# Optimization experiments

Hardware: AMD Instinct MI355X
Metric: run time of the kernel (lower is better)

The kernel has to match this reference:

```python
import jax, jax.numpy as jnp
import numpy as np

B, S, D = 4, 2048, 2048
H = 16
DH = D // H  # 128

def _rope_tables(seq_len, d_head, base=10000.0):
    inv_freq = 1.0 / (base ** (np.arange(0, d_head, 2, dtype=np.float32) / d_head))
    pos = np.arange(seq_len, dtype=np.float32)
    ang = pos[:, None] * inv_freq[None, :]  # (S, d_head/2)
    return jnp.asarray(np.cos(ang)), jnp.asarray(np.sin(ang))

def setup_inputs() -> dict:
    key = jax.random.key(0)
    ks = jax.random.split(key, 4)
    x = jax.random.normal(ks[0], (B, S, D), dtype=jnp.float32)
    rope_cos, rope_sin = _rope_tables(S, DH)
    # Linear params, scaled like torch default init (~1/sqrt(fan_in))
    Wqkv = jax.random.normal(ks[1], (D, 3 * D), dtype=jnp.float32) / np.sqrt(D)
    bqkv = jnp.zeros((3 * D,), dtype=jnp.float32)
    Wout = jax.random.normal(ks[2], (D, D), dtype=jnp.float32) / np.sqrt(D)
    bout = jnp.zeros((D,), dtype=jnp.float32)
    return {"x": x, "rope_cos": rope_cos, "rope_sin": rope_sin,
            "Wqkv": Wqkv, "bqkv": bqkv, "Wout": Wout, "bout": bout}

def _apply_rope(x, cos, sin):
    # x: (B, H, S, DH); cos/sin: (S, DH/2), broadcast over B,H
    x1 = x[..., 0::2]
    x2 = x[..., 1::2]
    out = jnp.stack([x1 * cos - x2 * sin, x1 * sin + x2 * cos], axis=-1)
    return out.reshape(*out.shape[:-2], -1)  # interleave back to (..., DH)

def reference(x, rope_cos, rope_sin, Wqkv, bqkv, Wout, bout):
    qkv = (x @ Wqkv + bqkv).reshape(B, S, 3, H, DH)
    qkv = jnp.transpose(qkv, (2, 0, 3, 1, 4))  # (3, B, H, S, DH)
    q, k, v = qkv[0], qkv[1], qkv[2]
    q = _apply_rope(q, rope_cos, rope_sin)
    k = _apply_rope(k, rope_cos, rope_sin)
    scale = 1.0 / np.sqrt(DH)
    scores = jnp.einsum('bhqd,bhkd->bhqk', q, k) * scale  # (B,H,S,S)
    causal = jnp.tril(jnp.ones((S, S), dtype=bool))
    scores = jnp.where(causal, scores, jnp.finfo(scores.dtype).min)
    attn = jax.nn.softmax(scores, axis=-1)
    out = jnp.einsum('bhqk,bhkd->bhqd', attn, v)  # (B,H,S,DH)
    out = jnp.transpose(out, (0, 2, 1, 3)).reshape(B, S, D)
    return out @ Wout + bout
```

## Files before the change

kernel.cpp:

```cpp
#include <hip/hip_runtime.h>
#include <hip/hip_bf16.h>
#include <math.h>

typedef __attribute__((ext_vector_type(8))) short bf16x8;
typedef __attribute__((ext_vector_type(4))) float f32x4;
typedef __attribute__((ext_vector_type(16))) float f32x16;
typedef __attribute__((ext_vector_type(8))) unsigned short u16x8;
typedef __attribute__((ext_vector_type(4))) unsigned short u16x4;

static constexpr int B = 4, S = 2048, D = 2048, H = 16, DH = 128;
static constexpr int N3 = 3 * D;
static constexpr int M = B * S;

__device__ __forceinline__ unsigned short f2bf(float f) {
  unsigned u = __float_as_uint(f);
  u += 0x7fffu + ((u >> 16) & 1u);
  return (unsigned short)(u >> 16);
}
__device__ __forceinline__ float bf2f(unsigned short b) {
  return __uint_as_float(((unsigned)b) << 16);
}

__global__ __launch_bounds__(256) void cvt_kernel(const float* __restrict__ in,
                                                  unsigned short* __restrict__ out) {
  size_t i = (size_t)blockIdx.x * 256 + threadIdx.x;
  f32x4 v = *(const f32x4*)(in + i * 4);
  u16x4 o;
  o[0] = f2bf(v[0]); o[1] = f2bf(v[1]); o[2] = f2bf(v[2]); o[3] = f2bf(v[3]);
  *(u16x4*)(out + i * 4) = o;
}

__global__ __launch_bounds__(256) void transpose_kernel(const float* __restrict__ W,
                                                        unsigned short* __restrict__ WT,
                                                        int K, int N) {
  __shared__ float t[32][33];
  int tx = threadIdx.x, ty = threadIdx.y;
  int n0 = blockIdx.x * 32, k0 = blockIdx.y * 32;
#pragma unroll
  for (int i = 0; i < 4; i++)
    t[ty + i * 8][tx] = W[(size_t)(k0 + ty + i * 8) * N + n0 + tx];
  __syncthreads();
#pragma unroll
  for (int i = 0; i < 4; i++)
    WT[(size_t)(n0 + ty + i * 8) * K + k0 + tx] = f2bf(t[tx][ty + i * 8]);
}

__device__ __forceinline__ void gload_lds(const void* g, void* l) {
  __builtin_amdgcn_global_load_lds((const __attribute__((address_space(1))) void*)g,
                                   (__attribute__((address_space(3))) void*)l, 16, 0, 0);
}

template <int EPI>
__global__ __launch_bounds__(512, 1) void gemm_bt(
    const unsigned short* __restrict__ A, const unsigned short* __restrict__ Bt,
    const float* __restrict__ bias, float* __restrict__ Cf,
    unsigned short* __restrict__ Qp, unsigned short* __restrict__ Kp,
    unsigned short* __restrict__ VTp, int Nn, int nbn) {
  __shared__ __align__(16) unsigned short lds[4 * 16384];
  constexpr int NT = 64;
  const int tid = threadIdx.x;
  const int l = tid & 63;
  const int w = tid >> 6;
  const int lr = l >> 4, lc = l & 15;
  const int wm = w >> 2, wn = w & 3;

  const int nwg = gridDim.x;
  const int cpx = nwg >> 3;
  const int wg = blockIdx.x;
  const int swz = (wg & 7) * cpx + (wg >> 3);
  const int bm = swz / nbn;
  const int bn = swz - bm * nbn;

  const unsigned short* Asrc[2];
  const unsigned short* Bsrc[2];
  int ldA[2], ldB[2];
#pragma unroll
  for (int i = 0; i < 2; i++) {
    const int gi = i * 512 + tid;
    const int r = gi >> 2, c = gi & 3;
    const int cs = c ^ ((r >> 1) & 3);
    Asrc[i] = A + (size_t)(bm * 256 + r) * 2048 + cs * 8;
    ldA[i] = gi * 8;
    Bsrc[i] = Bt + (size_t)(bn * 256 + r) * 2048 + cs * 8;
    ldB[i] = 8192 + gi * 8;
  }

  f32x4 acc[8][4];
#pragma unroll
  for (int m = 0; m < 8; m++)
#pragma unroll
    for (int n = 0; n < 4; n++) acc[m][n] = (f32x4)0.f;

  const int swzr = (lr ^ ((lc >> 1) & 3)) * 8;
  const int aoff = (wm * 128 + lc) * 32 + swzr;
  const int boff = 8192 + (wn * 64 + lc) * 32 + swzr;

#pragma unroll
  for (int t = 0; t < 3; t++) {
    unsigned short* sb = lds + t * 16384;
    gload_lds(Asrc[0] + t * 32, sb + ldA[0]);
    gload_lds(Asrc[1] + t * 32, sb + ldA[1]);
    gload_lds(Bsrc[0] + t * 32, sb + ldB[0]);
    gload_lds(Bsrc[1] + t * 32, sb + ldB[1]);
  }
  __builtin_amdgcn_sched_barrier(0);
  asm volatile("s_waitcnt vmcnt(8)" ::: "memory");
  __builtin_amdgcn_s_barrier();
  __builtin_amdgcn_sched_barrier(0);

  for (int kt = 0; kt < NT; kt++) {
    const unsigned short* buf = lds + (kt & 3) * 16384;
    unsigned short* sb = lds + ((kt + 3) & 3) * 16384;
    const bool stg = (kt + 3) < NT;
    const int ks = (kt + 3) * 32;
    bf16x8 a0[4], bb[4];
#pragma unroll
    for (int mf = 0; mf < 4; mf++) a0[mf] = *(const bf16x8*)(buf + aoff + mf * 512);
#pragma unroll
    for (int nf = 0; nf < 4; nf++) bb[nf] = *(const bf16x8*)(buf + boff + nf * 512);
    if (stg) { gload_lds(Asrc[0] + ks, sb + ldA[0]); gload_lds(Asrc[1] + ks, sb + ldA[1]); }
    __builtin_amdgcn_sched_barrier(0);
    __builtin_amdgcn_s_barrier();
    asm volatile("s_waitcnt lgkmcnt(0)" ::: "memory");
    __builtin_amdgcn_sched_barrier(0);
    __builtin_amdgcn_s_setprio(1);
#pragma unroll
    for (int m = 0; m < 4; m++)
#pragma unroll
      for (int n = 0; n < 4; n++)
        acc[m][n] = __builtin_amdgcn_mfma_f32_16x16x32_bf16(a0[m], bb[n], acc[m][n], 0, 0, 0);
    __builtin_amdgcn_s_setprio(0);
    __builtin_amdgcn_sched_barrier(0);
    __builtin_amdgcn_s_barrier();
    bf16x8 a1[4];
#pragma unroll
    for (int mf = 0; mf < 4; mf++) a1[mf] = *(const bf16x8*)(buf + aoff + (mf + 4) * 512);
    if (stg) { gload_lds(Bsrc[0] + ks, sb + ldB[0]); gload_lds(Bsrc[1] + ks, sb + ldB[1]); }
    __builtin_amdgcn_sched_barrier(0);
    __builtin_amdgcn_s_barrier();
    asm volatile("s_waitcnt lgkmcnt(0)" ::: "memory");
    __builtin_amdgcn_sched_barrier(0);
    __builtin_amdgcn_s_setprio(1);
#pragma unroll
    for (int m = 0; m < 4; m++)
#pragma unroll
      for (int n = 0; n < 4; n++)
        acc[m + 4][n] = __builtin_amdgcn_mfma_f32_16x16x32_bf16(a1[m], bb[n], acc[m + 4][n], 0, 0, 0);
    __builtin_amdgcn_s_setprio(0);
    __builtin_amdgcn_sched_barrier(0);
    if (kt + 3 < NT)      asm volatile("s_waitcnt vmcnt(8)" ::: "memory");
    else if (kt + 2 < NT) asm volatile("s_waitcnt vmcnt(4)" ::: "memory");
    else if (kt + 1 < NT) asm volatile("s_waitcnt vmcnt(0)" ::: "memory");
    __builtin_amdgcn_sched_barrier(0);
    __builtin_amdgcn_s_barrier();
    __builtin_amdgcn_sched_barrier(0);
  }

#pragma unroll
  for (int m = 0; m < 8; m++) {
#pragma unroll
    for (int n = 0; n < 4; n++) {
      const int col = bn * 256 + wn * 64 + n * 16 + lc;
      const float bv = bias[col];
#pragma unroll
      for (int r = 0; r < 4; r++) {
        const int row = bm * 256 + wm * 128 + m * 16 + lr * 4 + r;
        const float v = acc[m][n][r] + bv;
        if (EPI == 0) {
          const unsigned short ob = f2bf(v);
          const int b = row >> 11, s = row & 2047;
          const int which = col >> 11, within = col & 2047;
          const int h = within >> 7, d = within & 127;
          const size_t bh = (size_t)(b * H + h);
          if (which == 0)      Qp[(bh * S + s) * DH + d] = ob;
          else if (which == 1) Kp[(bh * S + s) * DH + d] = ob;
          else                 VTp[(bh * DH + d) * S + s] = ob;
        } else {
          Cf[(size_t)row * Nn + col] = v;
        }
      }
    }
  }
}

__global__ __launch_bounds__(256) void rope_kernel(unsigned short* __restrict__ T,
                                                   const float* __restrict__ cosT,
                                                   const float* __restrict__ sinT) {
  int t = blockIdx.x * 256 + threadIdx.x;
  int d8 = t & 15;
  int s = (t >> 4) & (S - 1);
  size_t off = (size_t)t * 8;
  u16x8 v = *(const u16x8*)(T + off);
  f32x4 c = *(const f32x4*)(cosT + (size_t)s * (DH / 2) + d8 * 4);
  f32x4 sn = *(const f32x4*)(sinT + (size_t)s * (DH / 2) + d8 * 4);
  u16x8 o;
#pragma unroll
  for (int j = 0; j < 4; j++) {
    float x1 = bf2f(v[2 * j]), x2 = bf2f(v[2 * j + 1]);
    o[2 * j]     = f2bf(x1 * c[j] - x2 * sn[j]);
    o[2 * j + 1] = f2bf(x1 * sn[j] + x2 * c[j]);
  }
  *(u16x8*)(T + off) = o;
}

__global__ __launch_bounds__(512, 1) void attn3_kernel(
    const unsigned short* __restrict__ Q, const unsigned short* __restrict__ Kt,
    const unsigned short* __restrict__ VT, unsigned short* __restrict__ O) {
  __shared__ __align__(16) unsigned short lK[2][32 * 128];
  __shared__ __align__(16) unsigned short lV[2][128 * 40];
  const int tid = threadIdx.x;
  const int w = tid >> 6;
  const int l = tid & 63;
  const int ql = l & 31;
  const int hi = l >> 5;
  const int j = blockIdx.x;
  const int bh = ((j >> 3) & 7) * 8 + (j & 7);
  const int pr = j >> 6;
  const int b = bh >> 4, h = bh & 15;
  const size_t base = (size_t)bh * S * DH;
  const float cl = 0.088388347648318447f * 1.44269504088896341f;

  const int kdst = (tid * 8) ^ (((tid >> 4) & 7) << 3);
  const unsigned short* Kgb = Kt + base;
  const int vdh = tid >> 2;
  const int vc = (tid & 3) * 8;
  const int vdst = vdh * 40 + vc;
  const unsigned short* Vgr = VT + ((size_t)bh * DH + vdh) * S;
  const int sfix = (ql & 7) << 3;

  for (int half = 0; half < 2; half++) {
    const int strip = half ? 7 - pr : pr;
    const int qw0 = strip * 256 + w * 32;

    bf16x8 qf[8];
    const unsigned short* qp = Q + base + (size_t)(qw0 + ql) * DH + hi * 8;
#pragma unroll
    for (int t = 0; t < 8; t++) qf[t] = *(const bf16x8*)(qp + t * 16);

    f32x16 acc[4];
#pragma unroll
    for (int mt = 0; mt < 4; mt++) acc[mt] = (f32x16)0.f;
    float m = -INFINITY, lsum = 0.f;

    const int ntb = 8 * (strip + 1);
    const int last = 8 * strip + w;

    {
      f32x4 kr = *(const f32x4*)(Kgb + tid * 8);
      f32x4 vr = *(const f32x4*)(Vgr + vc);
      *(f32x4*)(&lK[0][kdst]) = kr;
      *(f32x4*)(&lV[0][vdst]) = vr;
      __syncthreads();
    }

    for (int kb = 0; kb < ntb; kb++) {
      const int cur = kb & 1;
      const bool more = (kb + 1 < ntb);
      f32x4 kr, vr;
      if (more) {
        kr = *(const f32x4*)(Kgb + (size_t)(kb + 1) * 4096 + tid * 8);
        vr = *(const f32x4*)(Vgr + (kb + 1) * 32 + vc);
      }
      if (kb <= last) {
        const unsigned short* kbuf = lK[cur];
        const unsigned short* vbuf = lV[cur];
        f32x16 st0 = (f32x16)0.f, st1 = (f32x16)0.f;
#pragma unroll
        for (int t = 0; t < 4; t++) {
          bf16x8 k0 = *(const bf16x8*)(kbuf + ((ql * 128 + (2 * t) * 16 + 8 * hi) ^ sfix));
          bf16x8 k1 = *(const bf16x8*)(kbuf + ((ql * 128 + (2 * t + 1) * 16 + 8 * hi) ^ sfix));
          st0 = __builtin_amdgcn_mfma_f32_32x32x16_bf16(k0, qf[2 * t], st0, 0, 0, 0);
          st1 = __builtin_amdgcn_mfma_f32_32x32x16_bf16(k1, qf[2 * t + 1], st1, 0, 0, 0);
        }
        float sv[16];
#pragma unroll
        for (int r = 0; r < 16; r++) sv[r] = st0[r] + st1[r];
        if (kb == last) {
#pragma unroll
          for (int r = 0; r < 16; r++) {
            const int klocal = (r & 3) + 8 * (r >> 2) + 4 * hi;
            sv[r] = (klocal > ql) ? -INFINITY : sv[r];
          }
        }
        float smax = sv[0];
#pragma unroll
        for (int r = 1; r < 16; r++) smax = fmaxf(smax, sv[r]);
        smax = fmaxf(smax, __shfl_xor(smax, 32));

        float fr = 1.f;
        if (!__all((smax - m) * cl <= 8.0f)) {
          const float mn = fmaxf(m, smax);
          fr = exp2f((m - mn) * cl);
          m = mn;
#pragma unroll
          for (int mt = 0; mt < 4; mt++)
#pragma unroll
            for (int r = 0; r < 16; r++) acc[mt][r] *= fr;
        }
        float p[16];
        float ps = 0.f;
#pragma unroll
        for (int r = 0; r < 16; r++) {
          p[r] = exp2f((sv[r] - m) * cl);
          ps += p[r];
        }
        lsum = lsum * fr + ps + __shfl_xor(ps, 32);

        unsigned W[8];
#pragma unroll
        for (int qd = 0; qd < 4; qd++) {
          W[2 * qd]     = (unsigned)f2bf(p[4 * qd])     | ((unsigned)f2bf(p[4 * qd + 1]) << 16);
          W[2 * qd + 1] = (unsigned)f2bf(p[4 * qd + 2]) | ((unsigned)f2bf(p[4 * qd + 3]) << 16);
        }
#pragma unroll
        for (int t = 0; t < 2; t++) {
          const unsigned s0 = hi ? W[4 * t] : W[4 * t + 2];
          const unsigned s1 = hi ? W[4 * t + 1] : W[4 * t + 3];
          const unsigned r0 = __shfl_xor((int)s0, 32);
          const unsigned r1 = __shfl_xor((int)s1, 32);
          union { unsigned u[4]; bf16x8 v; } pf;
          if (hi == 0) { pf.u[0] = W[4 * t]; pf.u[1] = W[4 * t + 1]; pf.u[2] = r0; pf.u[3] = r1; }
          else         { pf.u[0] = r0; pf.u[1] = r1; pf.u[2] = W[4 * t + 2]; pf.u[3] = W[4 * t + 3]; }
#pragma unroll
          for (int mt = 0; mt < 4; mt++) {
            const bf16x8 vf = *(const bf16x8*)(vbuf + (mt * 32 + ql) * 40 + 16 * t + 8 * hi);
            acc[mt] = __builtin_amdgcn_mfma_f32_32x32x16_bf16(vf, pf.v, acc[mt], 0, 0, 0);
          }
        }
      }
      if (more) {
        *(f32x4*)(&lK[cur ^ 1][kdst]) = kr;
        *(f32x4*)(&lV[cur ^ 1][vdst]) = vr;
      }
      __syncthreads();
    }

    const float inv = 1.f / lsum;
    const int s_glob = qw0 + ql;
    unsigned short* op = O + ((size_t)(b * S + s_glob) * H + h) * DH;
#pragma unroll
    for (int mt = 0; mt < 4; mt++)
#pragma unroll
      for (int g = 0; g < 4; g++) {
        u16x4 ov;
#pragma unroll
        for (int jj = 0; jj < 4; jj++) ov[jj] = f2bf(acc[mt][4 * g + jj] * inv);
        *(u16x4*)(op + mt * 32 + 8 * g + 4 * hi) = ov;
      }
  }
}

extern "C" void kernel_launch(void* const* d_in, const int* in_sizes, int n_in,
                              void* d_out, int out_size, void* d_ws, size_t ws_size,
                              hipStream_t stream) {
  const float* x    = (const float*)d_in[0];
  const float* cosT = (const float*)d_in[1];
  const float* sinT = (const float*)d_in[2];
  const float* Wqkv = (const float*)d_in[3];
  const float* bqkv = (const float*)d_in[4];
  const float* Wout = (const float*)d_in[5];
  const float* bout = (const float*)d_in[6];

  char* ws = (char*)d_ws;
  unsigned short* xbf   = (unsigned short*)(ws);
  unsigned short* WqkvT = (unsigned short*)(ws + ((size_t)32 << 20));
  unsigned short* WoutT = (unsigned short*)(ws + ((size_t)56 << 20));
  unsigned short* VTb   = (unsigned short*)(ws + ((size_t)64 << 20));
  unsigned short* Qb = (unsigned short*)d_out;
  unsigned short* Kb = (unsigned short*)d_out + (size_t)M * D;
  unsigned short* Ob = xbf;

  cvt_kernel<<<M * D / 1024, 256, 0, stream>>>(x, xbf);
  transpose_kernel<<<dim3(N3 / 32, D / 32), dim3(32, 8), 0, stream>>>(Wqkv, WqkvT, D, N3);
  transpose_kernel<<<dim3(D / 32, D / 32), dim3(32, 8), 0, stream>>>(Wout, WoutT, D, D);
  gemm_bt<0><<<dim3((M / 256) * (N3 / 256)), 512, 0, stream>>>(xbf, WqkvT, bqkv, nullptr,
                                                               Qb, Kb, VTb, N3, N3 / 256);
  rope_kernel<<<(B * H * S * 16) / 256, 256, 0, stream>>>(Qb, cosT, sinT);
  rope_kernel<<<(B * H * S * 16) / 256, 256, 0, stream>>>(Kb, cosT, sinT);
  attn3_kernel<<<B * H * 4, 512, 0, stream>>>(Qb, Kb, VTb, Ob);
  gemm_bt<1><<<dim3((M / 256) * (D / 256)), 512, 0, stream>>>(Ob, WoutT, bout, (float*)d_out,
                                                              nullptr, nullptr, nullptr, D, D / 256);
}
```

Before: 502.2 us.

## Prefetch next k-tile LDS fragments into registers with ping-pong GEMM pipeline

Restructures the GEMM main loop so each iteration loads the next k-tile's A/B fragments from LDS into a second register set while MFMAs run on the current set. Partial lgkmcnt waits replace full drains, and the mid-iteration barriers are removed, leaving one barrier per tile. Global pointers are now advanced incrementally instead of recomputing offsets. This hides LDS read latency behind MFMA work at the cost of more VGPRs, and relies on fragile waitcnt and buffer-reuse ordering.

Result: faster. 490.0 us (-2.4%).

```diff
diff --git a/kernel.cpp b/kernel.cpp
--- a/kernel.cpp
+++ b/kernel.cpp
@@ -48,6 +48,60 @@
 __device__ __forceinline__ void gload_lds(const void* g, void* l) {
   __builtin_amdgcn_global_load_lds((const __attribute__((address_space(1))) void*)g,
                                    (__attribute__((address_space(3))) void*)l, 16, 0, 0);
+}
+
+template <bool NXT, bool STG, int VMN>
+__device__ __forceinline__ void gemm_tile(
+    const unsigned short* __restrict__ rb, unsigned short* __restrict__ sb,
+    bf16x8 (&CA)[8], bf16x8 (&CB)[4], bf16x8 (&NA)[8], bf16x8 (&NB)[4],
+    f32x4 (&acc)[8][4], int aoff, int boff,
+    const unsigned short*& pA0, const unsigned short*& pA1,
+    const unsigned short*& pB0, const unsigned short*& pB1,
+    int ldA0, int ldA1, int ldB0, int ldB1) {
+  if (NXT) {
+#pragma unroll
+    for (int mf = 0; mf < 4; mf++) NA[mf] = *(const bf16x8*)(rb + aoff + mf * 512);
+#pragma unroll
+    for (int nf = 0; nf < 4; nf++) NB[nf] = *(const bf16x8*)(rb + boff + nf * 512);
+  }
+  if (STG) { gload_lds(pA0, sb + ldA0); gload_lds(pA1, sb + ldA1); pA0 += 32; pA1 += 32; }
+  __builtin_amdgcn_sched_barrier(0);
+  if (NXT) asm volatile("s_waitcnt lgkmcnt(12)" ::: "memory");
+  else     asm volatile("s_waitcnt lgkmcnt(4)" ::: "memory");
+  __builtin_amdgcn_sched_barrier(0);
+  __builtin_amdgcn_s_setprio(1);
+#pragma unroll
+  for (int m = 0; m < 4; m++)
+#pragma unroll
+    for (int n = 0; n < 4; n++)
+      acc[m][n] = __builtin_amdgcn_mfma_f32_16x16x32_bf16(CA[m], CB[n], acc[m][n], 0, 0, 0);
+  __builtin_amdgcn_s_setprio(0);
+  __builtin_amdgcn_sched_barrier(0);
+  if (NXT) {
+#pragma unroll
+    for (int mf = 4; mf < 8; mf++) NA[mf] = *(const bf16x8*)(rb + aoff + mf * 512);
+  }
+  if (STG) { gload_lds(pB0, sb + ldB0); gload_lds(pB1, sb + ldB1); pB0 += 32; pB1 += 32; }
+  __builtin_amdgcn_sched_barrier(0);
+  if (NXT) asm volatile("s_waitcnt lgkmcnt(12)" ::: "memory");
+  else     asm volatile("s_waitcnt lgkmcnt(0)" ::: "memory");
+  __builtin_amdgcn_sched_barrier(0);
+  __builtin_amdgcn_s_setprio(1);
+#pragma unroll
+  for (int m = 0; m < 4; m++)
+#pragma unroll
+    for (int n = 0; n < 4; n++)
+      acc[m + 4][n] = __builtin_amdgcn_mfma_f32_16x16x32_bf16(CA[m + 4], CB[n], acc[m + 4][n], 0, 0, 0);
+  __builtin_amdgcn_s_setprio(0);
+  __builtin_amdgcn_sched_barrier(0);
+  if (VMN == 4) {
+    asm volatile("s_waitcnt vmcnt(4)" ::: "memory");
+    __builtin_amdgcn_s_barrier();
+  } else if (VMN == 0) {
+    asm volatile("s_waitcnt vmcnt(0)" ::: "memory");
+    __builtin_amdgcn_s_barrier();
+  }
+  __builtin_amdgcn_sched_barrier(0);
 }
 
 template <int EPI>
@@ -71,19 +125,15 @@
   const int bm = swz / nbn;
   const int bn = swz - bm * nbn;
 
-  const unsigned short* Asrc[2];
-  const unsigned short* Bsrc[2];
-  int ldA[2], ldB[2];
-#pragma unroll
-  for (int i = 0; i < 2; i++) {
-    const int gi = i * 512 + tid;
-    const int r = gi >> 2, c = gi & 3;
-    const int cs = c ^ ((r >> 1) & 3);
-    Asrc[i] = A + (size_t)(bm * 256 + r) * 2048 + cs * 8;
-    ldA[i] = gi * 8;
-    Bsrc[i] = Bt + (size_t)(bn * 256 + r) * 2048 + cs * 8;
-    ldB[i] = 8192 + gi * 8;
-  }
+  const int gi0 = tid, gi1 = 512 + tid;
+  const int r0 = gi0 >> 2, c0 = (gi0 & 3) ^ ((r0 >> 1) & 3);
+  const int r1 = gi1 >> 2, c1 = (gi1 & 3) ^ ((r1 >> 1) & 3);
+  const unsigned short* pA0 = A + (size_t)(bm * 256 + r0) * 2048 + c0 * 8;
+  const unsigned short* pA1 = A + (size_t)(bm * 256 + r1) * 2048 + c1 * 8;
+  const unsigned short* pB0 = Bt + (size_t)(bn * 256 + r0) * 2048 + c0 * 8;
+  const unsigned short* pB1 = Bt + (size_t)(bn * 256 + r1) * 2048 + c1 * 8;
+  const int ldA0 = gi0 * 8, ldA1 = gi1 * 8;
+  const int ldB0 = 8192 + gi0 * 8, ldB1 = 8192 + gi1 * 8;
 
   f32x4 acc[8][4];
 #pragma unroll
@@ -98,63 +148,44 @@
 #pragma unroll
   for (int t = 0; t < 3; t++) {
     unsigned short* sb = lds + t * 16384;
-    gload_lds(Asrc[0] + t * 32, sb + ldA[0]);
-    gload_lds(Asrc[1] + t * 32, sb + ldA[1]);
-    gload_lds(Bsrc[0] + t * 32, sb + ldB[0]);
-    gload_lds(Bsrc[1] + t * 32, sb + ldB[1]);
-  }
-  __builtin_amdgcn_sched_barrier(0);
-  asm volatile("s_waitcnt vmcnt(8)" ::: "memory");
+    gload_lds(pA0, sb + ldA0); gload_lds(pA1, sb + ldA1);
+    gload_lds(pB0, sb + ldB0); gload_lds(pB1, sb + ldB1);
+    pA0 += 32; pA1 += 32; pB0 += 32; pB1 += 32;
+  }
+  __builtin_amdgcn_sched_barrier(0);
+  asm volatile("s_waitcnt vmcnt(4)" ::: "memory");
   __builtin_amdgcn_s_barrier();
   __builtin_amdgcn_sched_barrier(0);
 
-  for (int kt = 0; kt < NT; kt++) {
-    const unsigned short* buf = lds + (kt & 3) * 16384;
-    unsigned short* sb = lds + ((kt + 3) & 3) * 16384;
-    const bool stg = (kt + 3) < NT;
-    const int ks = (kt + 3) * 32;
-    bf16x8 a0[4], bb[4];
-#pragma unroll
-    for (int mf = 0; mf < 4; mf++) a0[mf] = *(const bf16x8*)(buf + aoff + mf * 512);
-#pragma unroll
-    for (int nf = 0; nf < 4; nf++) bb[nf] = *(const bf16x8*)(buf + boff + nf * 512);
-    if (stg) { gload_lds(Asrc[0] + ks, sb + ldA[0]); gload_lds(Asrc[1] + ks, sb + ldA[1]); }
-    __builtin_amdgcn_sched_barrier(0);
-    __builtin_amdgcn_s_barrier();
-    asm volatile("s_waitcnt lgkmcnt(0)" ::: "memory");
-    __builtin_amdgcn_sched_barrier(0);
-    __builtin_amdgcn_s_setprio(1);
-#pragma unroll
-    for (int m = 0; m < 4; m++)
-#pragma unroll
-      for (int n = 0; n < 4; n++)
-        acc[m][n] = __builtin_amdgcn_mfma_f32_16x16x32_bf16(a0[m], bb[n], acc[m][n], 0, 0, 0);
-    __builtin_amdgcn_s_setprio(0);
-    __builtin_amdgcn_sched_barrier(0);
-    __builtin_amdgcn_s_barrier();
-    bf16x8 a1[4];
-#pragma unroll
-    for (int mf = 0; mf < 4; mf++) a1[mf] = *(const bf16x8*)(buf + aoff + (mf + 4) * 512);
-    if (stg) { gload_lds(Bsrc[0] + ks, sb + ldB[0]); gload_lds(Bsrc[1] + ks, sb + ldB[1]); }
-    __builtin_amdgcn_sched_barrier(0);
-    __builtin_amdgcn_s_barrier();
-    asm volatile("s_waitcnt lgkmcnt(0)" ::: "memory");
-    __builtin_amdgcn_sched_barrier(0);
-    __builtin_amdgcn_s_setprio(1);
-#pragma unroll
-    for (int m = 0; m < 4; m++)
-#pragma unroll
-      for (int n = 0; n < 4; n++)
-        acc[m + 4][n] = __builtin_amdgcn_mfma_f32_16x16x32_bf16(a1[m], bb[n], acc[m + 4][n], 0, 0, 0);
-    __builtin_amdgcn_s_setprio(0);
-    __builtin_amdgcn_sched_barrier(0);
-    if (kt + 3 < NT)      asm volatile("s_waitcnt vmcnt(8)" ::: "memory");
-    else if (kt + 2 < NT) asm volatile("s_waitcnt vmcnt(4)" ::: "memory");
-    else if (kt + 1 < NT) asm volatile("s_waitcnt vmcnt(0)" ::: "memory");
-    __builtin_amdgcn_sched_barrier(0);
-    __builtin_amdgcn_s_barrier();
-    __builtin_amdgcn_sched_barrier(0);
-  }
+  bf16x8 a0[8], b0[4], a1[8], b1[4];
+#pragma unroll
+  for (int mf = 0; mf < 4; mf++) a0[mf] = *(const bf16x8*)(lds + aoff + mf * 512);
+#pragma unroll
+  for (int nf = 0; nf < 4; nf++) b0[nf] = *(const bf16x8*)(lds + boff + nf * 512);
+#pragma unroll
+  for (int mf = 4; mf < 8; mf++) a0[mf] = *(const bf16x8*)(lds + aoff + mf * 512);
+  __builtin_amdgcn_sched_barrier(0);
+
+  for (int kt = 0; kt < 60; kt += 2) {
+    gemm_tile<true, true, 4>(lds + ((kt + 1) & 3) * 16384, lds + ((kt + 3) & 3) * 16384,
+                             a0, b0, a1, b1, acc, aoff, boff,
+                             pA0, pA1, pB0, pB1, ldA0, ldA1, ldB0, ldB1);
+    gemm_tile<true, true, 4>(lds + ((kt + 2) & 3) * 16384, lds + ((kt + 4) & 3) * 16384,
+                             a1, b1, a0, b0, acc, aoff, boff,
+                             pA0, pA1, pB0, pB1, ldA0, ldA1, ldB0, ldB1);
+  }
+  gemm_tile<true, true, 4>(lds + (61 & 3) * 16384, lds + (63 & 3) * 16384,
+                           a0, b0, a1, b1, acc, aoff, boff,
+                           pA0, pA1, pB0, pB1, ldA0, ldA1, ldB0, ldB1);
+  gemm_tile<true, false, 0>(lds + (62 & 3) * 16384, lds,
+                            a1, b1, a0, b0, acc, aoff, boff,
+                            pA0, pA1, pB0, pB1, ldA0, ldA1, ldB0, ldB1);
+  gemm_tile<true, false, -1>(lds + (63 & 3) * 16384, lds,
+                             a0, b0, a1, b1, acc, aoff, boff,
+                             pA0, pA1, pB0, pB1, ldA0, ldA1, ldB0, ldB1);
+  gemm_tile<false, false, -1>(lds, lds,
+                              a1, b1, a0, b0, acc, aoff, boff,
+                              pA0, pA1, pB0, pB1, ldA0, ldA1, ldB0, ldB1);
 
 #pragma unroll
   for (int m = 0; m < 8; m++) {
```
